# Kernel optimization log

Measured on AMD Instinct MI355X. Metric: run time of the kernel, lower is better.

## Reference

```python
import jax, jax.numpy as jnp
import numpy as np

DIM = 1024
HEADS = 16
SCALE = DIM ** -0.5  # NOTE: original uses full dim, not head dim


def setup_inputs() -> dict:
    key = jax.random.key(0)
    k1, k2, k3, k4 = jax.random.split(key, 4)
    x = jax.random.normal(k1, (2, 2048, DIM), dtype=jnp.float32)
    # torch nn.Linear(dim, 3*dim, bias=False): y = x @ W_qkv (stored here as [dim, 3*dim])
    w_qkv = jax.random.normal(k2, (DIM, 3 * DIM), dtype=jnp.float32) * (DIM ** -0.5)
    w_out = jax.random.normal(k3, (DIM, DIM), dtype=jnp.float32) * (DIM ** -0.5)
    b_out = jax.random.normal(k4, (DIM,), dtype=jnp.float32) * 0.01
    return {"x": x, "w_qkv": w_qkv, "w_out": w_out, "b_out": b_out}


def reference(x, w_qkv, w_out, b_out):
    b, n, d = x.shape
    h = HEADS
    hd = d // h
    qkv = x @ w_qkv  # [b, n, 3*d]
    # last dim layout is (qkv, h, hd) per rearrange 'b n (qkv h d) -> qkv b h n d'
    qkv = qkv.reshape(b, n, 3, h, hd)
    q, k, v = (jnp.moveaxis(qkv, (2, 3), (0, 2))[i] for i in range(3))  # each [b, h, n, hd]
    dots = jnp.einsum('bhid,bhjd->bhij', q, k) * SCALE
    causal_mask = jnp.triu(jnp.ones((n, n), dtype=bool), k=1)
    dots = jnp.where(causal_mask, -jnp.inf, dots)
    attn = jax.nn.softmax(dots, axis=-1)
    out = jnp.einsum('bhij,bhjd->bhid', attn, v)
    out = jnp.moveaxis(out, 1, 2).reshape(b, n, d)  # 'b h n d -> b n (h d)'
    return out @ w_out + b_out
```

## Files before the change

kernel.cpp:

```cpp
#include <hip/hip_runtime.h>

typedef __attribute__((ext_vector_type(8))) short bf16x8;
typedef __attribute__((ext_vector_type(4))) float f32x4;
typedef unsigned short u16;
typedef unsigned int u32;

#define SEQ 2048
#define NHEAD 16
#define EXP2_SCALE 0.045084219f

__device__ __forceinline__ u16 f2bf(float f){
  u32 u = __builtin_bit_cast(u32, f);
  u += 0x7FFFu + ((u >> 16) & 1u);
  return (u16)(u >> 16);
}

__device__ __forceinline__ void gl16(const u16* g, u16* l){
  __builtin_amdgcn_global_load_lds(
      (__attribute__((address_space(1))) void*)(unsigned long long)(const void*)g,
      (__attribute__((address_space(3))) void*)(unsigned)(unsigned long long)(const void*)l,
      16, 0, 0);
}

__global__ __launch_bounds__(256) void prep(const float* __restrict__ x,
                                            const float* __restrict__ w_qkv,
                                            const float* __restrict__ w_out,
                                            u16* __restrict__ xb,
                                            u16* __restrict__ wqkvT,
                                            u16* __restrict__ woutT){
  __shared__ u16 t[32][33];
  const int bid = blockIdx.x;
  if (bid < 4096){
    int i = (bid * 256 + threadIdx.x) << 2;
    float4 v = *(const float4*)&x[i];
    ushort4 o;
    o.x = f2bf(v.x); o.y = f2bf(v.y); o.z = f2bf(v.z); o.w = f2bf(v.w);
    *(ushort4*)&xb[i] = o;
    return;
  }
  const float* src; u16* dst; int R, C, bx, by;
  if (bid < 7168){ int tt = bid - 4096; src = w_qkv; dst = wqkvT; R = 1024; C = 3072; bx = tt % 96; by = tt / 96; }
  else           { int tt = bid - 7168; src = w_out; dst = woutT; R = 1024; C = 1024; bx = tt % 32; by = tt / 32; }
  const int c0 = bx << 5, r0 = by << 5;
  const int tx = threadIdx.x & 31, tg = threadIdx.x >> 5;
  #pragma unroll
  for (int i = 0; i < 4; i++){
    int r = (tg << 2) + i;
    t[r][tx] = f2bf(src[(size_t)(r0 + r) * C + (c0 + tx)]);
  }
  __syncthreads();
  #pragma unroll
  for (int i = 0; i < 4; i++){
    int c = (tg << 2) + i;
    dst[(size_t)(c0 + c) * R + (r0 + tx)] = t[tx][c];
  }
}

__global__ __launch_bounds__(256) void gemm_qkv(const u16* __restrict__ A,
                                                const u16* __restrict__ Bt,
                                                u16* __restrict__ Qo,
                                                u16* __restrict__ Ko,
                                                u16* __restrict__ Vto){
  __shared__ u16 As[128 * 64];
  __shared__ u16 Bs[128 * 64];
  const int tid = threadIdx.x;
  const int lane = tid & 63, wid = tid >> 6;
  const int l15 = lane & 15, quad = lane >> 4;
  const int wm = wid >> 1, wn = wid & 1;
  const int bid = blockIdx.x;
  const int xcd = bid & 7, t8 = bid >> 3;
  const int bm = ((xcd << 2) + (t8 & 3)) << 7;
  const int bn = (t8 >> 2) << 7;
  const int qkv_idx = bn >> 10;

  const int lr = lane >> 3;
  const int cc = (lane & 7) ^ lr;
  const u16* gA0 = A  + (size_t)(bm + wid * 32 + lr) * 1024 + (cc << 3);
  const u16* gB0 = Bt + (size_t)(bn + wid * 32 + lr) * 1024 + (cc << 3);
  u16* lA0 = &As[wid * 2048];
  u16* lB0 = &Bs[wid * 2048];

  f32x4 acc[4][4];
  #pragma unroll
  for (int i = 0; i < 4; i++)
    #pragma unroll
    for (int j = 0; j < 4; j++) acc[i][j] = (f32x4){0.f, 0.f, 0.f, 0.f};

  for (int k0 = 0; k0 < 1024; k0 += 64){
    #pragma unroll
    for (int t = 0; t < 4; t++){
      gl16(gA0 + k0 + t * 8192, lA0 + t * 512);
      gl16(gB0 + k0 + t * 8192, lB0 + t * 512);
    }
    __syncthreads();
    #pragma unroll
    for (int hf = 0; hf < 2; hf++){
      bf16x8 af[4], bfr[4];
      #pragma unroll
      for (int mt = 0; mt < 4; mt++){
        int row = wm * 64 + mt * 16 + l15;
        af[mt] = *(const bf16x8*)&As[row * 64 + (((hf * 4 + quad) ^ (row & 7)) << 3)];
      }
      #pragma unroll
      for (int nt = 0; nt < 4; nt++){
        int row = wn * 64 + nt * 16 + l15;
        bfr[nt] = *(const bf16x8*)&Bs[row * 64 + (((hf * 4 + quad) ^ (row & 7)) << 3)];
      }
      #pragma unroll
      for (int mt = 0; mt < 4; mt++)
        #pragma unroll
        for (int nt = 0; nt < 4; nt++)
          acc[mt][nt] = __builtin_amdgcn_mfma_f32_16x16x32_bf16(bfr[nt], af[mt], acc[mt][nt], 0, 0, 0);
    }
    __syncthreads();
  }

  if (qkv_idx != 2){
    const float qs = (qkv_idx == 0) ? EXP2_SCALE : 1.0f;
    u16* dst = (qkv_idx == 0) ? Qo : Ko;
    #pragma unroll
    for (int mt = 0; mt < 4; mt++){
      int xr = bm + wm * 64 + mt * 16 + l15;
      int b = xr >> 11, pos = xr & 2047;
      #pragma unroll
      for (int nt = 0; nt < 4; nt++){
        int c0 = bn + wn * 64 + nt * 16 + quad * 4;
        int head = (c0 & 1023) >> 6, hd0 = c0 & 63;
        size_t bhh = ((size_t)(b * NHEAD + head)) << 17;
        ushort4 w;
        w.x = f2bf(acc[mt][nt][0] * qs); w.y = f2bf(acc[mt][nt][1] * qs);
        w.z = f2bf(acc[mt][nt][2] * qs); w.w = f2bf(acc[mt][nt][3] * qs);
        *(ushort4*)&dst[bhh + ((size_t)pos << 6) + hd0] = w;
      }
    }
  } else {
    #pragma unroll
    for (int mt = 0; mt < 4; mt++){
      int xr = bm + wm * 64 + mt * 16 + l15;
      int b = xr >> 11, pos = xr & 2047;
      #pragma unroll
      for (int nt = 0; nt < 4; nt++){
        #pragma unroll
        for (int r = 0; r < 4; r++){
          int c = bn + wn * 64 + nt * 16 + quad * 4 + r;
          int head = (c & 1023) >> 6, hd_i = c & 63;
          size_t bhh = ((size_t)(b * NHEAD + head)) << 17;
          Vto[bhh + ((size_t)hd_i << 11) + pos] = f2bf(acc[mt][nt][r]);
        }
      }
    }
  }
}

__global__ __launch_bounds__(256) void attn_kernel(const u16* __restrict__ Q,
                                                   const u16* __restrict__ K,
                                                   const u16* __restrict__ Vt,
                                                   u16* __restrict__ Oo){
  __shared__ u16 Ks[128 * 64];
  __shared__ u16 Vts[64 * 128];
  __shared__ u16 Ps[4][16 * 136];
  const int tid = threadIdx.x;
  const int lane = tid & 63, wid = tid >> 6;
  const int l15 = lane & 15, quad = lane >> 4;
  const int bh = blockIdx.x & 31;
  const int qt = 31 - (blockIdx.x >> 5);
  const size_t base = ((size_t)bh) << 17;
  const int b = bh >> 4, h = bh & 15;

  const u16* qsrc = Q + base + ((size_t)((qt << 6) + wid * 16 + l15) << 6) + quad * 8;
  const bf16x8 bq0 = *(const bf16x8*)qsrc;
  const bf16x8 bq1 = *(const bf16x8*)(qsrc + 32);

  const int rK = wid * 32 + (lane >> 3);
  const int cK = (lane & 7) ^ (rK & 7);
  const u16* gK0 = K + base + ((size_t)rK << 6) + (cK << 3);
  u16* lK = &Ks[wid * 2048];
  const u16* gV[4];
  #pragma unroll
  for (int t = 0; t < 4; t++){
    int rv = wid * 16 + t * 4 + (lane >> 4);
    int cv = (lane & 15) ^ (rv & 15);
    gV[t] = Vt + base + (size_t)rv * 2048 + (cv << 3);
  }
  u16* lV = &Vts[wid * 2048];

  f32x4 o[4];
  #pragma unroll
  for (int dt = 0; dt < 4; dt++) o[dt] = (f32x4){0.f, 0.f, 0.f, 0.f};
  float lsum = 0.f;
  const int qpos = (qt << 6) + wid * 16 + l15;
  const int jt_max = qt >> 1;
  u16* Pw = &Ps[wid][0];

  auto kv_iter = [&](const int jt, const bool diag) __attribute__((always_inline)) {
    const u16* gk = gK0 + (size_t)jt * 8192;
    #pragma unroll
    for (int t = 0; t < 4; t++) gl16(gk + t * 512, lK + t * 512);
    #pragma unroll
    for (int t = 0; t < 4; t++) gl16(gV[t] + (jt << 7), lV + t * 512);
    __syncthreads();

    f32x4 st[8];
    #pragma unroll
    for (int mt = 0; mt < 8; mt++) st[mt] = (f32x4){0.f, 0.f, 0.f, 0.f};
    #pragma unroll
    for (int mt = 0; mt < 8; mt++){
      int kvr = mt * 16 + l15;
      bf16x8 ak0 = *(const bf16x8*)&Ks[kvr * 64 + ((quad ^ (kvr & 7)) << 3)];
      st[mt] = __builtin_amdgcn_mfma_f32_16x16x32_bf16(ak0, bq0, st[mt], 0, 0, 0);
      bf16x8 ak1 = *(const bf16x8*)&Ks[kvr * 64 + (((4 + quad) ^ (kvr & 7)) << 3)];
      st[mt] = __builtin_amdgcn_mfma_f32_16x16x32_bf16(ak1, bq1, st[mt], 0, 0, 0);
    }

    #pragma unroll
    for (int mt = 0; mt < 8; mt++){
      float pr[4];
      #pragma unroll
      for (int r = 0; r < 4; r++){
        float w = st[mt][r];
        if (diag){
          int kv = (jt << 7) + mt * 16 + quad * 4 + r;
          if (kv > qpos) w = -INFINITY;
        }
        pr[r] = __builtin_amdgcn_exp2f(w);
      }
      lsum += (pr[0] + pr[1]) + (pr[2] + pr[3]);
      u32 a0 = __builtin_bit_cast(u32, pr[0]) + 0x8000u;
      u32 a1 = __builtin_bit_cast(u32, pr[1]) + 0x8000u;
      u32 a2 = __builtin_bit_cast(u32, pr[2]) + 0x8000u;
      u32 a3 = __builtin_bit_cast(u32, pr[3]) + 0x8000u;
      uint2 pk;
      pk.x = __builtin_amdgcn_perm(a1, a0, 0x07060302u);
      pk.y = __builtin_amdgcn_perm(a3, a2, 0x07060302u);
      *(uint2*)&Pw[l15 * 136 + mt * 16 + quad * 4] = pk;
    }

    #pragma unroll
    for (int ks = 0; ks < 4; ks++){
      bf16x8 bp = *(const bf16x8*)&Pw[l15 * 136 + ks * 32 + quad * 8];
      #pragma unroll
      for (int dt = 0; dt < 4; dt++){
        int dr = dt * 16 + l15;
        bf16x8 av = *(const bf16x8*)&Vts[dr * 128 + (((ks * 4 + quad) ^ (dr & 15)) << 3)];
        o[dt] = __builtin_amdgcn_mfma_f32_16x16x32_bf16(av, bp, o[dt], 0, 0, 0);
      }
    }
    __syncthreads();
  };

  for (int jt = 0; jt < jt_max; jt++) kv_iter(jt, false);
  kv_iter(jt_max, true);

  lsum += __shfl_xor(lsum, 16);
  lsum += __shfl_xor(lsum, 32);
  float inv = 1.f / lsum;
  const size_t orow = (size_t)((b << 11) + qpos) * 1024 + h * 64;
  #pragma unroll
  for (int dt = 0; dt < 4; dt++){
    ushort4 w;
    w.x = f2bf(o[dt][0] * inv); w.y = f2bf(o[dt][1] * inv);
    w.z = f2bf(o[dt][2] * inv); w.w = f2bf(o[dt][3] * inv);
    *(ushort4*)&Oo[orow + dt * 16 + quad * 4] = w;
  }
}

__global__ __launch_bounds__(256) void gemm_out(const u16* __restrict__ A,
                                                const u16* __restrict__ Bt,
                                                const float* __restrict__ bias,
                                                float* __restrict__ out){
  __shared__ u16 As[128 * 64];
  __shared__ u16 Bs[128 * 64];
  const int tid = threadIdx.x;
  const int lane = tid & 63, wid = tid >> 6;
  const int l15 = lane & 15, quad = lane >> 4;
  const int wm = wid >> 1, wn = wid & 1;
  const int bid = blockIdx.x;
  const int xcd = bid & 7, t8 = bid >> 3;
  const int bm = ((xcd << 2) + (t8 & 3)) << 7;
  const int bn = (t8 >> 2) << 7;

  const int lr = lane >> 3;
  const int cc = (lane & 7) ^ lr;
  const u16* gA0 = A  + (size_t)(bm + wid * 32 + lr) * 1024 + (cc << 3);
  const u16* gB0 = Bt + (size_t)(bn + wid * 32 + lr) * 1024 + (cc << 3);
  u16* lA0 = &As[wid * 2048];
  u16* lB0 = &Bs[wid * 2048];

  f32x4 acc[4][4];
  #pragma unroll
  for (int i = 0; i < 4; i++)
    #pragma unroll
    for (int j = 0; j < 4; j++) acc[i][j] = (f32x4){0.f, 0.f, 0.f, 0.f};

  for (int k0 = 0; k0 < 1024; k0 += 64){
    #pragma unroll
    for (int t = 0; t < 4; t++){
      gl16(gA0 + k0 + t * 8192, lA0 + t * 512);
      gl16(gB0 + k0 + t * 8192, lB0 + t * 512);
    }
    __syncthreads();
    #pragma unroll
    for (int hf = 0; hf < 2; hf++){
      bf16x8 af[4], bfr[4];
      #pragma unroll
      for (int mt = 0; mt < 4; mt++){
        int row = wm * 64 + mt * 16 + l15;
        af[mt] = *(const bf16x8*)&As[row * 64 + (((hf * 4 + quad) ^ (row & 7)) << 3)];
      }
      #pragma unroll
      for (int nt = 0; nt < 4; nt++){
        int row = wn * 64 + nt * 16 + l15;
        bfr[nt] = *(const bf16x8*)&Bs[row * 64 + (((hf * 4 + quad) ^ (row & 7)) << 3)];
      }
      #pragma unroll
      for (int mt = 0; mt < 4; mt++)
        #pragma unroll
        for (int nt = 0; nt < 4; nt++)
          acc[mt][nt] = __builtin_amdgcn_mfma_f32_16x16x32_bf16(bfr[nt], af[mt], acc[mt][nt], 0, 0, 0);
    }
    __syncthreads();
  }

  #pragma unroll
  for (int nt = 0; nt < 4; nt++){
    int c0 = bn + wn * 64 + nt * 16 + quad * 4;
    float4 bv = *(const float4*)&bias[c0];
    #pragma unroll
    for (int mt = 0; mt < 4; mt++){
      int row = bm + wm * 64 + mt * 16 + l15;
      float4 w;
      w.x = acc[mt][nt][0] + bv.x; w.y = acc[mt][nt][1] + bv.y;
      w.z = acc[mt][nt][2] + bv.z; w.w = acc[mt][nt][3] + bv.w;
      *(float4*)&out[(size_t)row * 1024 + c0] = w;
    }
  }
}

extern "C" void kernel_launch(void* const* d_in, const int* in_sizes, int n_in,
                              void* d_out, int out_size, void* d_ws, size_t ws_size,
                              hipStream_t stream){
  const float* x     = (const float*)d_in[0];
  const float* w_qkv = (const float*)d_in[1];
  const float* w_out = (const float*)d_in[2];
  const float* b_out = (const float*)d_in[3];
  float* out = (float*)d_out;

  char* ws = (char*)d_ws;
  u16* xb    = (u16*)(ws);
  u16* wqkvT = (u16*)(ws + (8u  << 20));
  u16* woutT = (u16*)(ws + (14u << 20));
  u16* Qb    = (u16*)(ws + (16u << 20));
  u16* Kb    = (u16*)(ws + (24u << 20));
  u16* Vtb   = (u16*)(ws + (32u << 20));
  u16* attn  = (u16*)(ws + (40u << 20));

  prep<<<8192, 256, 0, stream>>>(x, w_qkv, w_out, xb, wqkvT, woutT);
  gemm_qkv<<<768, 256, 0, stream>>>(xb, wqkvT, Qb, Kb, Vtb);
  attn_kernel<<<dim3(1024), 256, 0, stream>>>(Qb, Kb, Vtb, attn);
  gemm_out<<<256, 256, 0, stream>>>(attn, woutT, b_out, out);
}
```

Measured before the change: 176.6 us.

## Switch attention kernel to 32x32x16 MFMA with register-resident P via lane shuffles

```diff
diff --git a/kernel.cpp b/kernel.cpp
--- a/kernel.cpp
+++ b/kernel.cpp
@@ -2,6 +2,7 @@
 
 typedef __attribute__((ext_vector_type(8))) short bf16x8;
 typedef __attribute__((ext_vector_type(4))) float f32x4;
+typedef __attribute__((ext_vector_type(16))) float f32x16;
 typedef unsigned short u16;
 typedef unsigned int u32;
 
@@ -152,97 +153,118 @@
   }
 }
 
-__global__ __launch_bounds__(256) void attn_kernel(const u16* __restrict__ Q,
+__global__ __launch_bounds__(128) void attn_kernel(const u16* __restrict__ Q,
                                                    const u16* __restrict__ K,
                                                    const u16* __restrict__ Vt,
                                                    u16* __restrict__ Oo){
   __shared__ u16 Ks[128 * 64];
   __shared__ u16 Vts[64 * 128];
-  __shared__ u16 Ps[4][16 * 136];
   const int tid = threadIdx.x;
   const int lane = tid & 63, wid = tid >> 6;
-  const int l15 = lane & 15, quad = lane >> 4;
+  const int l31 = lane & 31, h = lane >> 5;
+  const bool hb = (h != 0);
   const int bh = blockIdx.x & 31;
   const int qt = 31 - (blockIdx.x >> 5);
   const size_t base = ((size_t)bh) << 17;
-  const int b = bh >> 4, h = bh & 15;
-
-  const u16* qsrc = Q + base + ((size_t)((qt << 6) + wid * 16 + l15) << 6) + quad * 8;
-  const bf16x8 bq0 = *(const bf16x8*)qsrc;
-  const bf16x8 bq1 = *(const bf16x8*)(qsrc + 32);
-
-  const int rK = wid * 32 + (lane >> 3);
-  const int cK = (lane & 7) ^ (rK & 7);
-  const u16* gK0 = K + base + ((size_t)rK << 6) + (cK << 3);
-  u16* lK = &Ks[wid * 2048];
+  const int b = bh >> 4, head = bh & 15;
+
+  const int qpos = (qt << 6) + wid * 32 + l31;
+  const u16* qsrc = Q + base + ((size_t)qpos << 6) + h * 8;
+  bf16x8 bq[4];
+  #pragma unroll
+  for (int ks = 0; ks < 4; ks++) bq[ks] = *(const bf16x8*)(qsrc + ks * 16);
+
+  const int lrK = lane >> 3;
+  const int cK = (lane & 7) ^ lrK;
+  const u16* gK0 = K + base + ((size_t)(wid * 64 + lrK) << 6) + (cK << 3);
+  u16* lK = &Ks[wid * 4096];
   const u16* gV[4];
   #pragma unroll
   for (int t = 0; t < 4; t++){
-    int rv = wid * 16 + t * 4 + (lane >> 4);
+    int rv = wid * 32 + t * 4 + (lane >> 4);
     int cv = (lane & 15) ^ (rv & 15);
     gV[t] = Vt + base + (size_t)rv * 2048 + (cv << 3);
   }
-  u16* lV = &Vts[wid * 2048];
-
-  f32x4 o[4];
-  #pragma unroll
-  for (int dt = 0; dt < 4; dt++) o[dt] = (f32x4){0.f, 0.f, 0.f, 0.f};
+  u16* lV = &Vts[wid * 4096];
+
+  f32x16 o[2];
+  #pragma unroll
+  for (int i = 0; i < 2; i++)
+    #pragma unroll
+    for (int r = 0; r < 16; r++) o[i][r] = 0.f;
   float lsum = 0.f;
-  const int qpos = (qt << 6) + wid * 16 + l15;
   const int jt_max = qt >> 1;
-  u16* Pw = &Ps[wid][0];
 
   auto kv_iter = [&](const int jt, const bool diag) __attribute__((always_inline)) {
     const u16* gk = gK0 + (size_t)jt * 8192;
     #pragma unroll
-    for (int t = 0; t < 4; t++) gl16(gk + t * 512, lK + t * 512);
-    #pragma unroll
-    for (int t = 0; t < 4; t++) gl16(gV[t] + (jt << 7), lV + t * 512);
-    __syncthreads();
-
-    f32x4 st[8];
-    #pragma unroll
-    for (int mt = 0; mt < 8; mt++) st[mt] = (f32x4){0.f, 0.f, 0.f, 0.f};
-    #pragma unroll
-    for (int mt = 0; mt < 8; mt++){
-      int kvr = mt * 16 + l15;
-      bf16x8 ak0 = *(const bf16x8*)&Ks[kvr * 64 + ((quad ^ (kvr & 7)) << 3)];
-      st[mt] = __builtin_amdgcn_mfma_f32_16x16x32_bf16(ak0, bq0, st[mt], 0, 0, 0);
-      bf16x8 ak1 = *(const bf16x8*)&Ks[kvr * 64 + (((4 + quad) ^ (kvr & 7)) << 3)];
-      st[mt] = __builtin_amdgcn_mfma_f32_16x16x32_bf16(ak1, bq1, st[mt], 0, 0, 0);
-    }
-
-    #pragma unroll
-    for (int mt = 0; mt < 8; mt++){
-      float pr[4];
-      #pragma unroll
-      for (int r = 0; r < 4; r++){
-        float w = st[mt][r];
-        if (diag){
-          int kv = (jt << 7) + mt * 16 + quad * 4 + r;
-          if (kv > qpos) w = -INFINITY;
-        }
-        pr[r] = __builtin_amdgcn_exp2f(w);
-      }
-      lsum += (pr[0] + pr[1]) + (pr[2] + pr[3]);
-      u32 a0 = __builtin_bit_cast(u32, pr[0]) + 0x8000u;
-      u32 a1 = __builtin_bit_cast(u32, pr[1]) + 0x8000u;
-      u32 a2 = __builtin_bit_cast(u32, pr[2]) + 0x8000u;
-      u32 a3 = __builtin_bit_cast(u32, pr[3]) + 0x8000u;
-      uint2 pk;
-      pk.x = __builtin_amdgcn_perm(a1, a0, 0x07060302u);
-      pk.y = __builtin_amdgcn_perm(a3, a2, 0x07060302u);
-      *(uint2*)&Pw[l15 * 136 + mt * 16 + quad * 4] = pk;
-    }
-
-    #pragma unroll
-    for (int ks = 0; ks < 4; ks++){
-      bf16x8 bp = *(const bf16x8*)&Pw[l15 * 136 + ks * 32 + quad * 8];
-      #pragma unroll
-      for (int dt = 0; dt < 4; dt++){
-        int dr = dt * 16 + l15;
-        bf16x8 av = *(const bf16x8*)&Vts[dr * 128 + (((ks * 4 + quad) ^ (dr & 15)) << 3)];
-        o[dt] = __builtin_amdgcn_mfma_f32_16x16x32_bf16(av, bp, o[dt], 0, 0, 0);
+    for (int t = 0; t < 8; t++) gl16(gk + t * 512, lK + t * 512);
+    #pragma unroll
+    for (int t = 0; t < 8; t++) gl16(gV[t & 3] + (t >> 2) * 32768 + (jt << 7), lV + t * 512);
+    __syncthreads();
+
+    #pragma unroll
+    for (int mtp = 0; mtp < 4; mtp += 2){
+      f32x16 st[2];
+      #pragma unroll
+      for (int u = 0; u < 2; u++)
+        #pragma unroll
+        for (int r = 0; r < 16; r++) st[u][r] = 0.f;
+      #pragma unroll
+      for (int ks = 0; ks < 4; ks++){
+        #pragma unroll
+        for (int u = 0; u < 2; u++){
+          int row = (mtp + u) * 32 + l31;
+          bf16x8 ak = *(const bf16x8*)&Ks[row * 64 + (((ks * 2 + h) ^ (row & 7)) << 3)];
+          st[u] = __builtin_amdgcn_mfma_f32_32x32x16_bf16(ak, bq[ks], st[u], 0, 0, 0);
+        }
+      }
+      #pragma unroll
+      for (int u = 0; u < 2; u++){
+        const int mt = mtp + u;
+        float pr[16];
+        #pragma unroll
+        for (int r = 0; r < 16; r++){
+          float w = st[u][r];
+          if (diag){
+            int kv = (jt << 7) + mt * 32 + (r & 3) + 8 * (r >> 2) + 4 * h;
+            if (kv > qpos) w = -INFINITY;
+          }
+          pr[r] = __builtin_amdgcn_exp2f(w);
+          lsum += pr[r];
+        }
+        u32 pk[8];
+        #pragma unroll
+        for (int g = 0; g < 4; g++){
+          u32 a0 = __builtin_bit_cast(u32, pr[4*g+0]) + 0x8000u;
+          u32 a1 = __builtin_bit_cast(u32, pr[4*g+1]) + 0x8000u;
+          u32 a2 = __builtin_bit_cast(u32, pr[4*g+2]) + 0x8000u;
+          u32 a3 = __builtin_bit_cast(u32, pr[4*g+3]) + 0x8000u;
+          pk[2*g]   = __builtin_amdgcn_perm(a1, a0, 0x07060302u);
+          pk[2*g+1] = __builtin_amdgcn_perm(a3, a2, 0x07060302u);
+        }
+        #pragma unroll
+        for (int half = 0; half < 2; half++){
+          u32 A0 = pk[4*half+0], A1 = pk[4*half+1];
+          u32 B0 = pk[4*half+2], B1 = pk[4*half+3];
+          u32 sA0 = (u32)__shfl_xor((int)A0, 32);
+          u32 sA1 = (u32)__shfl_xor((int)A1, 32);
+          u32 sB0 = (u32)__shfl_xor((int)B0, 32);
+          u32 sB1 = (u32)__shfl_xor((int)B1, 32);
+          uint4 wv;
+          wv.x = hb ? sB0 : A0;
+          wv.y = hb ? sB1 : A1;
+          wv.z = hb ? B0  : sA0;
+          wv.w = hb ? B1  : sA1;
+          bf16x8 bp = __builtin_bit_cast(bf16x8, wv);
+          const int s = mt * 2 + half;
+          #pragma unroll
+          for (int dt = 0; dt < 2; dt++){
+            int dr = dt * 32 + l31;
+            bf16x8 av = *(const bf16x8*)&Vts[dr * 128 + (((s * 2 + h) ^ (dr & 15)) << 3)];
+            o[dt] = __builtin_amdgcn_mfma_f32_32x32x16_bf16(av, bp, o[dt], 0, 0, 0);
+          }
+        }
       }
     }
     __syncthreads();
@@ -251,16 +273,18 @@
   for (int jt = 0; jt < jt_max; jt++) kv_iter(jt, false);
   kv_iter(jt_max, true);
 
-  lsum += __shfl_xor(lsum, 16);
   lsum += __shfl_xor(lsum, 32);
   float inv = 1.f / lsum;
-  const size_t orow = (size_t)((b << 11) + qpos) * 1024 + h * 64;
-  #pragma unroll
-  for (int dt = 0; dt < 4; dt++){
-    ushort4 w;
-    w.x = f2bf(o[dt][0] * inv); w.y = f2bf(o[dt][1] * inv);
-    w.z = f2bf(o[dt][2] * inv); w.w = f2bf(o[dt][3] * inv);
-    *(ushort4*)&Oo[orow + dt * 16 + quad * 4] = w;
+  const size_t orow = (size_t)((b << 11) + qpos) * 1024 + head * 64;
+  #pragma unroll
+  for (int dt = 0; dt < 2; dt++){
+    #pragma unroll
+    for (int g = 0; g < 4; g++){
+      ushort4 w;
+      w.x = f2bf(o[dt][4*g+0] * inv); w.y = f2bf(o[dt][4*g+1] * inv);
+      w.z = f2bf(o[dt][4*g+2] * inv); w.w = f2bf(o[dt][4*g+3] * inv);
+      *(ushort4*)&Oo[orow + dt * 32 + 8 * g + 4 * h] = w;
+    }
   }
 }
 
@@ -356,6 +380,6 @@
 
   prep<<<8192, 256, 0, stream>>>(x, w_qkv, w_out, xb, wqkvT, woutT);
   gemm_qkv<<<768, 256, 0, stream>>>(xb, wqkvT, Qb, Kb, Vtb);
-  attn_kernel<<<dim3(1024), 256, 0, stream>>>(Qb, Kb, Vtb, attn);
+  attn_kernel<<<dim3(1024), 128, 0, stream>>>(Qb, Kb, Vtb, attn);
   gemm_out<<<256, 256, 0, stream>>>(attn, woutT, b_out, out);
 }
```

New measurement: 182.8 us. +3.5%, slower.
